# Performance work log

Hardware: AMD Instinct MI355X
Metric: run time of the kernel (lower is better)

## Reference

```python
import jax, jax.numpy as jnp
import numpy as np

N = 100000
E = 1600000
IN_C = 128
HID = 32
HEADS = 4
OUT_C = 16
G = 128
NEG_SLOPE = 0.2


def setup_inputs() -> dict:
    key = jax.random.key(0)
    ks = jax.random.split(key, 16)
    x = jax.random.normal(ks[0], (N, IN_C), dtype=jnp.float32)
    edge_index = jax.random.randint(ks[1], (2, E), 0, N, dtype=jnp.int64)
    batch = jnp.sort(jax.random.randint(ks[2], (N,), 0, G, dtype=jnp.int64))
    node_weights = jax.random.uniform(ks[3], (N, 1), dtype=jnp.float32)
    s = 1.0 / np.sqrt(IN_C)
    W1 = jax.random.uniform(ks[4], (IN_C, HEADS * HID), jnp.float32, -s, s)
    att_src1 = jax.random.uniform(ks[5], (HEADS, HID), jnp.float32, -s, s)
    att_dst1 = jax.random.uniform(ks[6], (HEADS, HID), jnp.float32, -s, s)
    b1 = jnp.zeros((HEADS * HID,), jnp.float32)
    s2 = 1.0 / np.sqrt(HEADS * HID)
    W2 = jax.random.uniform(ks[7], (HEADS * HID, HID), jnp.float32, -s2, s2)
    att_src2 = jax.random.uniform(ks[8], (1, HID), jnp.float32, -s2, s2)
    att_dst2 = jax.random.uniform(ks[9], (1, HID), jnp.float32, -s2, s2)
    b2 = jnp.zeros((HID,), jnp.float32)
    s3 = 1.0 / np.sqrt(HID)
    fcW = jax.random.uniform(ks[10], (HID, OUT_C), jnp.float32, -s3, s3)
    fcb = jax.random.uniform(ks[11], (OUT_C,), jnp.float32, -s3, s3)
    return {"x": x, "edge_index": edge_index, "batch": batch,
            "node_weights": node_weights,
            "W1": W1, "att_src1": att_src1, "att_dst1": att_dst1, "b1": b1,
            "W2": W2, "att_src2": att_src2, "att_dst2": att_dst2, "b2": b2,
            "fcW": fcW, "fcb": fcb}


def gat_conv(x, src, dst, W, att_src, att_dst, bias, heads, ch, concat):
    n = x.shape[0]
    h = (x @ W).reshape(n, heads, ch)                       # [N,H,C]
    a_src = jnp.sum(h * att_src[None], axis=-1)             # [N,H]
    a_dst = jnp.sum(h * att_dst[None], axis=-1)             # [N,H]
    e = jax.nn.leaky_relu(a_src[src] + a_dst[dst], NEG_SLOPE)  # [E,H]
    # segment softmax over incoming edges of each destination node
    e_max = jax.ops.segment_max(e, dst, num_segments=n)
    ex = jnp.exp(e - e_max[dst])
    denom = jax.ops.segment_sum(ex, dst, num_segments=n)
    alpha = ex / denom[dst]                                 # [E,H]
    msg = h[src] * alpha[..., None]                         # [E,H,C]
    out = jax.ops.segment_sum(msg, dst, num_segments=n)     # [N,H,C]
    if concat:
        out = out.reshape(n, heads * ch)
    else:
        out = out.mean(axis=1)
    return out + bias


def reference(x, edge_index, batch, node_weights,
              W1, att_src1, att_dst1, b1,
              W2, att_src2, att_dst2, b2,
              fcW, fcb):
    n = x.shape[0]
    # PyG GATConv adds self-loops by default
    loop = jnp.arange(n, dtype=edge_index.dtype)
    src = jnp.concatenate([edge_index[0], loop])
    dst = jnp.concatenate([edge_index[1], loop])

    h = x * node_weights
    h = jax.nn.elu(gat_conv(h, src, dst, W1, att_src1, att_dst1, b1, HEADS, HID, True))
    h = jax.nn.elu(gat_conv(h, src, dst, W2, att_src2, att_dst2, b2, 1, HID, False))
    # global mean pool over graphs
    sums = jax.ops.segment_sum(h, batch, num_segments=G)
    cnts = jax.ops.segment_sum(jnp.ones((n,), h.dtype), batch, num_segments=G)
    pooled = sums / jnp.maximum(cnts, 1.0)[:, None]
    return pooled @ fcW + fcb
```

## Files before the change

### kernel.cpp

```cpp
#include <hip/hip_runtime.h>
#include <cstdint>

#define NGRAPH 128
#define NEG 0.2f
#define NB_MAX 512
#define BSH 8
#define BSZ 256
#define CAP 8192

typedef unsigned int uint;
typedef unsigned short ushort;
typedef unsigned char uchar;
typedef __attribute__((ext_vector_type(8))) short bf16x8;
typedef __attribute__((ext_vector_type(4))) float f32x4;
typedef __attribute__((ext_vector_type(2))) float f32x2;

union U4B { uint4 u; bf16x8 v; };

__device__ __forceinline__ ushort f2bf(float f) {
  uint u = __float_as_uint(f);
  uint r = (u + 0x7FFF + ((u >> 16) & 1)) >> 16;
  return (ushort)r;
}

__device__ __forceinline__ uint cvtpkbf16(float lo, float hi) {
  uint r;
  asm("v_cvt_pk_bf16_f32 %0, %1, %2" : "=v"(r) : "v"(lo), "v"(hi));
  return r;
}

__device__ __forceinline__ void pkfma(f32x2& acc, f32x2 f, f32x2 w) {
  asm("v_pk_fma_f32 %0, %1, %2, %0" : "+v"(acc) : "v"(f), "v"(w));
}

__device__ __forceinline__ int wave_incl_scan_i(int v) {
  int lane = threadIdx.x & 63;
#pragma unroll
  for (int off = 1; off < 64; off <<= 1) {
    int u = __shfl_up(v, off, 64);
    if (lane >= off) v += u;
  }
  return v;
}

__global__ void k_bin(const int* __restrict__ ei,
                      const float* __restrict__ W1, const float* __restrict__ W2,
                      ushort* __restrict__ Wt1, ushort* __restrict__ Wt2,
                      int E, int Etot, int NB, int nbin,
                      int* __restrict__ bcur, uint* __restrict__ bbuf) {
  if (blockIdx.x >= (uint)nbin) {
    int t2 = (blockIdx.x - nbin) * 256 + threadIdx.x;
    if (t2 < 16384) {
      int n = t2 >> 7, k = t2 & 127;
      Wt1[t2] = f2bf(W1[k * 128 + n]);
    } else {
      int u = t2 - 16384;
      int n = u >> 7, k = u & 127;
      Wt2[u] = f2bf(W2[k * 32 + n]);
    }
    return;
  }
  __shared__ int h[NB_MAX];
  __shared__ int baseo[NB_MAX];
  int t = threadIdx.x;
  for (int b = t; b < NB; b += 256) h[b] = 0;
  __syncthreads();
  int cbase = blockIdx.x * 4096;
  int cend = min(cbase + 4096, Etot);
  for (int e = cbase + t; e < cend; e += 256) {
    int d = (e < E) ? ei[E + e] : (e - E);
    atomicAdd(&h[d >> BSH], 1);
  }
  __syncthreads();
  for (int b = t; b < NB; b += 256) {
    int c = h[b];
    baseo[b] = c ? atomicAdd(&bcur[b], c) : 0;
    h[b] = 0;
  }
  __syncthreads();
  for (int e = cbase + t; e < cend; e += 256) {
    int s, d;
    if (e < E) { s = ei[e]; d = ei[E + e]; } else { s = e - E; d = s; }
    int b = d >> BSH;
    int r = atomicAdd(&h[b], 1);
    bbuf[(size_t)b * CAP + baseo[b] + r] = ((uint)(d & (BSZ - 1)) << 17) | (uint)s;
  }
}

__global__ void k_bg(const uint* __restrict__ bbuf, const int* __restrict__ bcur,
                     int NB, int N, int* __restrict__ offs, int* __restrict__ ssrc,
                     const float* __restrict__ x, const ushort* __restrict__ Wt,
                     const float* __restrict__ nw, const float* __restrict__ att_s,
                     const float* __restrict__ att_d, uchar* __restrict__ hb1,
                     float* __restrict__ asrc, float* __restrict__ adst) {
  __shared__ int sst[NB_MAX + 1];
  __shared__ int wsum2[4];
  __shared__ int deg[BSZ];
  if (blockIdx.x < (uint)NB) {
    int t = threadIdx.x, lane = t & 63, wid = t >> 6;
    int v0 = (2 * t < NB) ? bcur[2 * t] : 0;
    int v1 = (2 * t + 1 < NB) ? bcur[2 * t + 1] : 0;
    int s = v0 + v1;
    int sv = wave_incl_scan_i(s);
    if (lane == 63) wsum2[wid] = sv;
    deg[t] = 0;
    __syncthreads();
    if (t == 0) {
      int r = 0;
#pragma unroll
      for (int k = 0; k < 4; k++) { int x2 = wsum2[k]; wsum2[k] = r; r += x2; }
    }
    __syncthreads();
    int excl = wsum2[wid] + sv - s;
    sst[2 * t] = excl;
    sst[2 * t + 1] = excl + v0;
    if (t == 255) sst[512] = excl + v0 + v1;
    __syncthreads();
    int b = blockIdx.x;
    int ebeg = sst[b], eend = sst[b + 1];
    int cnt = eend - ebeg;
    for (int i = t; i < cnt; i += BSZ)
      atomicAdd(&deg[bbuf[(size_t)b * CAP + i] >> 17], 1);
    __syncthreads();
    int v = deg[t];
    int sv2 = wave_incl_scan_i(v);
    if (lane == 63) wsum2[wid] = sv2;
    __syncthreads();
    if (t == 0) {
      int r = 0;
#pragma unroll
      for (int k = 0; k < 4; k++) { int x2 = wsum2[k]; wsum2[k] = r; r += x2; }
    }
    __syncthreads();
    int excl2 = wsum2[wid] + sv2 - v;
    int node = (b << BSH) + t;
    if (node < N) offs[node] = ebeg + excl2;
    if (b == 0 && t == 0) offs[N] = sst[512];
    __syncthreads();
    deg[t] = excl2;
    __syncthreads();
    for (int i = t; i < cnt; i += BSZ) {
      uint rec = bbuf[(size_t)b * CAP + i];
      int r = atomicAdd(&deg[rec >> 17], 1);
      ssrc[ebeg + r] = (int)(rec & 0x1FFFF);
    }
    return;
  }
  int bid = blockIdx.x - NB;
  int wv = threadIdx.x >> 6, l = threadIdx.x & 63;
  int lg = l >> 4, lr = l & 15;
  int row0 = bid * 64 + wv * 16;
  int node = row0 + lr;
  bool valid = node < N;
  float sc = valid ? nw[node] : 0.f;
  bf16x8 xfr[4];
  const float* xr = x + (size_t)node * 128;
#pragma unroll
  for (int kc = 0; kc < 4; kc++) {
    float v[8];
    if (valid) {
      float4 q0 = *reinterpret_cast<const float4*>(xr + kc * 32 + lg * 8);
      float4 q1 = *reinterpret_cast<const float4*>(xr + kc * 32 + lg * 8 + 4);
      v[0] = q0.x; v[1] = q0.y; v[2] = q0.z; v[3] = q0.w;
      v[4] = q1.x; v[5] = q1.y; v[6] = q1.z; v[7] = q1.w;
    } else {
#pragma unroll
      for (int j = 0; j < 8; j++) v[j] = 0.f;
    }
    U4B a;
    a.u.x = cvtpkbf16(v[0] * sc, v[1] * sc);
    a.u.y = cvtpkbf16(v[2] * sc, v[3] * sc);
    a.u.z = cvtpkbf16(v[4] * sc, v[5] * sc);
    a.u.w = cvtpkbf16(v[6] * sc, v[7] * sc);
    xfr[kc] = a.v;
  }
  float pS[4] = {}, pD[4] = {};
#pragma unroll
  for (int ct = 0; ct < 8; ct++) {
    f32x4 acc = {0.f, 0.f, 0.f, 0.f};
    const ushort* wrow = Wt + (size_t)(ct * 16 + lr) * 128;
#pragma unroll
    for (int kc = 0; kc < 4; kc++) {
      U4B bfr;
      bfr.u = *reinterpret_cast<const uint4*>(wrow + kc * 32 + lg * 8);
      acc = __builtin_amdgcn_mfma_f32_16x16x32_bf16(bfr.v, xfr[kc], acc, 0, 0, 0);
    }
    int c0 = ct * 16 + lg * 4;
    if (valid) {
      uint u8 = (uint)__builtin_amdgcn_cvt_pk_fp8_f32(acc[0], acc[1], 0, false);
      u8 = (uint)__builtin_amdgcn_cvt_pk_fp8_f32(acc[2], acc[3], u8, true);
      *reinterpret_cast<uint*>(hb1 + (size_t)node * 128 + c0) = u8;
    }
    float4 as4 = *reinterpret_cast<const float4*>(att_s + c0);
    float4 ad4 = *reinterpret_cast<const float4*>(att_d + c0);
    int h = ct >> 1;
    pS[h] += acc[0] * as4.x + acc[1] * as4.y + acc[2] * as4.z + acc[3] * as4.w;
    pD[h] += acc[0] * ad4.x + acc[1] * ad4.y + acc[2] * ad4.z + acc[3] * ad4.w;
  }
#pragma unroll
  for (int off = 16; off < 64; off <<= 1) {
#pragma unroll
    for (int h = 0; h < 4; h++) {
      pS[h] += __shfl_xor(pS[h], off, 64);
      pD[h] += __shfl_xor(pD[h], off, 64);
    }
  }
  if (lg == 0 && valid) {
    *reinterpret_cast<float4*>(asrc + node * 4) = make_float4(pS[0], pS[1], pS[2], pS[3]);
    *reinterpret_cast<float4*>(adst + node * 4) = make_float4(pD[0], pD[1], pD[2], pD[3]);
  }
}

__global__ void k_aggr1(const int* __restrict__ offs, const int* __restrict__ ssrc,
                        const uchar* __restrict__ hb, const float* __restrict__ asrc,
                        const float* __restrict__ adst, const float* __restrict__ bias,
                        const ushort* __restrict__ Wt2, const float* __restrict__ as2,
                        const float* __restrict__ ad2, uchar* __restrict__ hb2,
                        float* __restrict__ asrc2, float* __restrict__ adst2, int N) {
  __shared__ ushort rowl[4][136];
  int tid = threadIdx.x;
  int wv = tid >> 6, l = tid & 63;
  int d = blockIdx.x * 4 + wv;
  int dc = min(d, N - 1);
  int slot = l >> 3;
  int cb = l & 7;
  int h = cb >> 1;
  float ad = adst[dc * 4 + h];
  int beg = offs[dc], end = offs[dc + 1];
  int endm1 = end - 1;
  const uchar* hbc = hb + cb * 16;
  f32x2 a2[8] = {};
  float ds = 0.f;
  for (int i = beg; i < end; i += 8) {
    int e = i + slot;
    int ec = min(e, endm1);
    int s = ssrc[ec];
    float xv = asrc[s * 4 + h] + ad;
    xv = fmaxf(xv, xv * NEG);
    float w = __expf(xv);
    w = (e < end) ? w : 0.f;
    uint4 p = *reinterpret_cast<const uint4*>(hbc + (size_t)s * 128);
    f32x2 wp = {w, w};
    f32x2 f;
    f = __builtin_amdgcn_cvt_pk_f32_fp8(p.x, false); pkfma(a2[0], f, wp);
    f = __builtin_amdgcn_cvt_pk_f32_fp8(p.x, true);  pkfma(a2[1], f, wp);
    f = __builtin_amdgcn_cvt_pk_f32_fp8(p.y, false); pkfma(a2[2], f, wp);
    f = __builtin_amdgcn_cvt_pk_f32_fp8(p.y, true);  pkfma(a2[3], f, wp);
    f = __builtin_amdgcn_cvt_pk_f32_fp8(p.z, false); pkfma(a2[4], f, wp);
    f = __builtin_amdgcn_cvt_pk_f32_fp8(p.z, true);  pkfma(a2[5], f, wp);
    f = __builtin_amdgcn_cvt_pk_f32_fp8(p.w, false); pkfma(a2[6], f, wp);
    f = __builtin_amdgcn_cvt_pk_f32_fp8(p.w, true);  pkfma(a2[7], f, wp);
    ds += w;
  }
  int b3 = (l >> 3) & 1, b4 = (l >> 4) & 1, b5 = (l >> 5) & 1;
  float t8[8];
#pragma unroll
  for (int r = 0; r < 8; r++) {
    float av = a2[r >> 1][r & 1];
    float bv = a2[(r + 8) >> 1][r & 1];
    float send = b3 ? av : bv;
    float recv = __shfl_xor(send, 8, 64);
    t8[r] = (b3 ? bv : av) + recv;
  }
  float t4[4];
#pragma unroll
  for (int r = 0; r < 4; r++) {
    float send = b4 ? t8[r] : t8[r + 4];
    float recv = __shfl_xor(send, 16, 64);
    t4[r] = (b4 ? t8[r + 4] : t8[r]) + recv;
  }
  float t2[2];
#pragma unroll
  for (int r = 0; r < 2; r++) {
    float send = b5 ? t4[r] : t4[r + 2];
    float recv = __shfl_xor(send, 32, 64);
    t2[r] = (b5 ? t4[r + 2] : t4[r]) + recv;
  }
  ds += __shfl_xor(ds, 8, 64);
  ds += __shfl_xor(ds, 16, 64);
  ds += __shfl_xor(ds, 32, 64);
  float inv = __builtin_amdgcn_rcpf(ds > 0.f ? ds : 1.f);
  int c0 = cb * 16 + b3 * 8 + b4 * 4 + b5 * 2;
  float2 bi = *reinterpret_cast<const float2*>(bias + c0);
  float r0 = fmaf(t2[0], inv, bi.x);
  float r1 = fmaf(t2[1], inv, bi.y);
  r0 = r0 > 0.f ? r0 : __expf(r0) - 1.f;
  r1 = r1 > 0.f ? r1 : __expf(r1) - 1.f;
  *reinterpret_cast<uint*>(&rowl[wv][c0]) = cvtpkbf16(r0, r1);
  __syncthreads();
  if (wv != 0) return;
  int lg = l >> 4, lr = l & 15;
  int rsel = lr & 3;
  bf16x8 bfrag[4];
#pragma unroll
  for (int kc = 0; kc < 4; kc++) {
    U4B bb;
    bb.u = *reinterpret_cast<const uint4*>(&rowl[rsel][kc * 32 + lg * 8]);
    bfrag[kc] = bb.v;
  }
  int dd = blockIdx.x * 4 + lr;
  bool vs = (lr < 4) && (dd < N);
  float pS = 0.f, pD = 0.f;
#pragma unroll
  for (int ct = 0; ct < 2; ct++) {
    f32x4 acc = {0.f, 0.f, 0.f, 0.f};
    const ushort* wrow = Wt2 + (size_t)(ct * 16 + lr) * 128;
#pragma unroll
    for (int kc = 0; kc < 4; kc++) {
      U4B bfr;
      bfr.u = *reinterpret_cast<const uint4*>(wrow + kc * 32 + lg * 8);
      acc = __builtin_amdgcn_mfma_f32_16x16x32_bf16(bfr.v, bfrag[kc], acc, 0, 0, 0);
    }
    int cg = ct * 16 + lg * 4;
    if (vs) {
      uint u8 = (uint)__builtin_amdgcn_cvt_pk_fp8_f32(acc[0], acc[1], 0, false);
      u8 = (uint)__builtin_amdgcn_cvt_pk_fp8_f32(acc[2], acc[3], u8, true);
      *reinterpret_cast<uint*>(hb2 + (size_t)dd * 32 + cg) = u8;
    }
    float4 as4 = *reinterpret_cast<const float4*>(as2 + cg);
    float4 ad4 = *reinterpret_cast<const float4*>(ad2 + cg);
    pS += acc[0] * as4.x + acc[1] * as4.y + acc[2] * as4.z + acc[3] * as4.w;
    pD += acc[0] * ad4.x + acc[1] * ad4.y + acc[2] * ad4.z + acc[3] * ad4.w;
  }
  pS += __shfl_xor(pS, 16, 64);
  pS += __shfl_xor(pS, 32, 64);
  pD += __shfl_xor(pD, 16, 64);
  pD += __shfl_xor(pD, 32, 64);
  if (vs && lg == 0) { asrc2[dd] = pS; adst2[dd] = pD; }
}

__global__ void k_aggr2(const int* __restrict__ offs, const int* __restrict__ ssrc,
                        const uchar* __restrict__ hb, const float* __restrict__ asrc,
                        const float* __restrict__ adst, const float* __restrict__ bias,
                        float* __restrict__ out, int N) {
  int wid = threadIdx.x >> 6, l = threadIdx.x & 63;
  int d = blockIdx.x * 4 + wid;
  if (d >= N) return;
  int slot = l >> 2;
  int k = l & 3;
  float ad = adst[d];
  int beg = offs[d], end = offs[d + 1];
  int endm1 = end - 1;
  const uchar* hbc = hb + k * 8;
  f32x2 a2[4] = {};
  float ds = 0.f;
  for (int i = beg; i < end; i += 16) {
    int e = i + slot;
    int ec = min(e, endm1);
    int s = ssrc[ec];
    float xv = asrc[s] + ad;
    xv = fmaxf(xv, xv * NEG);
    float w = __expf(xv);
    w = (e < end) ? w : 0.f;
    uint2 p = *reinterpret_cast<const uint2*>(hbc + (size_t)s * 32);
    f32x2 wp = {w, w};
    f32x2 f;
    f = __builtin_amdgcn_cvt_pk_f32_fp8(p.x, false); pkfma(a2[0], f, wp);
    f = __builtin_amdgcn_cvt_pk_f32_fp8(p.x, true);  pkfma(a2[1], f, wp);
    f = __builtin_amdgcn_cvt_pk_f32_fp8(p.y, false); pkfma(a2[2], f, wp);
    f = __builtin_amdgcn_cvt_pk_f32_fp8(p.y, true);  pkfma(a2[3], f, wp);
    ds += w;
  }
  int b2 = (l >> 2) & 1, b3 = (l >> 3) & 1, b4 = (l >> 4) & 1;
  float t4[4];
#pragma unroll
  for (int r = 0; r < 4; r++) {
    float av = a2[r >> 1][r & 1];
    float bv = a2[(r + 4) >> 1][r & 1];
    float send = b2 ? av : bv;
    float recv = __shfl_xor(send, 4, 64);
    t4[r] = (b2 ? bv : av) + recv;
  }
  float t2[2];
#pragma unroll
  for (int r = 0; r < 2; r++) {
    float send = b3 ? t4[r] : t4[r + 2];
    float recv = __shfl_xor(send, 8, 64);
    t2[r] = (b3 ? t4[r + 2] : t4[r]) + recv;
  }
  float send = b4 ? t2[0] : t2[1];
  float recv = __shfl_xor(send, 16, 64);
  float t1 = (b4 ? t2[1] : t2[0]) + recv;
  t1 += __shfl_xor(t1, 32, 64);
  ds += __shfl_xor(ds, 4, 64);
  ds += __shfl_xor(ds, 8, 64);
  ds += __shfl_xor(ds, 16, 64);
  ds += __shfl_xor(ds, 32, 64);
  if (l < 32) {
    int c = k * 8 + b2 * 4 + b3 * 2 + b4;
    float inv = __builtin_amdgcn_rcpf(ds > 0.f ? ds : 1.f);
    float r = fmaf(t1, inv, bias[c]);
    r = r > 0.f ? r : __expf(r) - 1.f;
    out[(size_t)d * 32 + c] = r;
  }
}

__global__ void k_pool_fc(const float* __restrict__ h2, const int* __restrict__ batch,
                          const float* __restrict__ fcW, const float* __restrict__ fcb,
                          float* __restrict__ out, int N) {
  int g = blockIdx.x;
  int lo = 0, hi = N;
  while (lo < hi) { int mid = (lo + hi) >> 1; if (batch[mid] < g) lo = mid + 1; else hi = mid; }
  int beg = lo;
  hi = N;
  while (lo < hi) { int mid = (lo + hi) >> 1; if (batch[mid] < g + 1) lo = mid + 1; else hi = mid; }
  int end = lo;
  int t = threadIdx.x, c = t & 31, sub = t >> 5;
  float acc = 0.f;
  for (int n = beg + sub; n < end; n += 8) acc += h2[(size_t)n * 32 + c];
  __shared__ float red[8][32];
  __shared__ float pooled[32];
  red[sub][c] = acc;
  __syncthreads();
  if (sub == 0) {
    float s = 0.f;
#pragma unroll
    for (int i = 0; i < 8; i++) s += red[i][c];
    float cnt = (float)(end - beg);
    pooled[c] = s / fmaxf(cnt, 1.f);
  }
  __syncthreads();
  if (t < 16) {
    float r = fcb[t];
#pragma unroll
    for (int cc = 0; cc < 32; cc++) r += pooled[cc] * fcW[cc * 16 + t];
    out[g * 16 + t] = r;
  }
}

extern "C" void kernel_launch(void* const* d_in, const int* in_sizes, int n_in,
                              void* d_out, int out_size, void* d_ws, size_t ws_size,
                              hipStream_t stream) {
  const float* x     = (const float*)d_in[0];
  const int*   ei    = (const int*)d_in[1];
  const int*   batch = (const int*)d_in[2];
  const float* nw    = (const float*)d_in[3];
  const float* W1    = (const float*)d_in[4];
  const float* as1w  = (const float*)d_in[5];
  const float* ad1w  = (const float*)d_in[6];
  const float* b1    = (const float*)d_in[7];
  const float* W2    = (const float*)d_in[8];
  const float* as2w  = (const float*)d_in[9];
  const float* ad2w  = (const float*)d_in[10];
  const float* b2    = (const float*)d_in[11];
  const float* fcW   = (const float*)d_in[12];
  const float* fcb   = (const float*)d_in[13];
  float* out = (float*)d_out;

  const int N = in_sizes[0] / 128;
  const int E = in_sizes[1] / 2;
  const int Etot = E + N;
  const int NB = (N + BSZ - 1) >> BSH;

  char* w = (char*)d_ws;
  size_t ofs = 0;
  auto alloc = [&](size_t bytes) {
    char* p = w + ofs;
    ofs += (bytes + 255) & ~(size_t)255;
    return p;
  };
  uchar*  hb1    = (uchar*)alloc((size_t)N * 128);
  uchar*  hb2    = (uchar*)alloc((size_t)N * 32);
  float*  h2     = (float*)alloc((size_t)N * 32 * 4);
  float*  asrc1  = (float*)alloc((size_t)N * 4 * 4);
  float*  adst1  = (float*)alloc((size_t)N * 4 * 4);
  float*  asrc2  = (float*)alloc((size_t)N * 4);
  float*  adst2  = (float*)alloc((size_t)N * 4);
  ushort* Wt1    = (ushort*)alloc(16384 * 2);
  ushort* Wt2    = (ushort*)alloc(4096 * 2);
  int*    bcur   = (int*)alloc((size_t)NB * 4);
  int*    offs   = (int*)alloc((size_t)(N + 1) * 4);
  uint*   bbuf   = (uint*)alloc((size_t)NB * CAP * 4);
  int*    ssrc   = (int*)alloc((size_t)Etot * 4);

  hipMemsetAsync(bcur, 0, (size_t)NB * 4, stream);

  const int nbin = (Etot + 4095) / 4096;
  k_bin<<<nbin + 80, 256, 0, stream>>>(ei, W1, W2, Wt1, Wt2, E, Etot, NB, nbin, bcur, bbuf);

  const int ngemm1 = (N + 63) / 64;
  k_bg<<<NB + ngemm1, 256, 0, stream>>>(bbuf, bcur, NB, N, offs, ssrc,
                                        x, Wt1, nw, as1w, ad1w, hb1, asrc1, adst1);

  k_aggr1<<<(N + 3) / 4, 256, 0, stream>>>(offs, ssrc, hb1, asrc1, adst1, b1,
                                           Wt2, as2w, ad2w, hb2, asrc2, adst2, N);

  k_aggr2<<<(N + 3) / 4, 256, 0, stream>>>(offs, ssrc, hb2, asrc2, adst2, b2, h2, N);

  k_pool_fc<<<NGRAPH, 256, 0, stream>>>(h2, batch, fcW, fcb, out, N);
}
```

Baseline: 308.9 us.

## Compute edge weights once per edge and broadcast via ds_bpermute in aggregation

Both aggregation kernels now load source indices and compute the leaky-relu and exp attention weight once per edge per head, using dedicated lanes. The weights and indices are then broadcast to the lanes that do the feature gathers with ds_bpermute, instead of every lane redundantly loading ssrc/asrc and computing exp. Each iteration processes 32 (layer 1) or 64 (layer 2) edges, with up to four gathers in flight per lane. This removes redundant scalar loads and transcendental work and raises memory-level parallelism, at the cost of extra LDS permute traffic and branches for the tail chunks.

After: 305.1 us. About the same (-1.2%).

```diff
diff --git a/kernel.cpp b/kernel.cpp
--- a/kernel.cpp
+++ b/kernel.cpp
@@ -31,6 +31,13 @@
 
 __device__ __forceinline__ void pkfma(f32x2& acc, f32x2 f, f32x2 w) {
   asm("v_pk_fma_f32 %0, %1, %2, %0" : "+v"(acc) : "v"(f), "v"(w));
+}
+
+__device__ __forceinline__ float bperm_f(int addr, float v) {
+  return __int_as_float(__builtin_amdgcn_ds_bpermute(addr, __float_as_int(v)));
+}
+__device__ __forceinline__ int bperm_i(int addr, int v) {
+  return __builtin_amdgcn_ds_bpermute(addr, v);
 }
 
 __device__ __forceinline__ int wave_incl_scan_i(int v) {
@@ -225,21 +232,17 @@
   int slot = l >> 3;
   int cb = l & 7;
   int h = cb >> 1;
-  float ad = adst[dc * 4 + h];
+  int hq = l & 3;
+  int eidx = l >> 2;
+  float adq = adst[dc * 4 + hq];
   int beg = offs[dc], end = offs[dc + 1];
   int endm1 = end - 1;
   const uchar* hbc = hb + cb * 16;
+  int bp0 = (slot * 4 + h) << 2;
+  int bp1 = bp0 + 128;
   f32x2 a2[8] = {};
-  float ds = 0.f;
-  for (int i = beg; i < end; i += 8) {
-    int e = i + slot;
-    int ec = min(e, endm1);
-    int s = ssrc[ec];
-    float xv = asrc[s * 4 + h] + ad;
-    xv = fmaxf(xv, xv * NEG);
-    float w = __expf(xv);
-    w = (e < end) ? w : 0.f;
-    uint4 p = *reinterpret_cast<const uint4*>(hbc + (size_t)s * 128);
+  float dsp = 0.f;
+  auto ACC = [&](uint4 p, float w) {
     f32x2 wp = {w, w};
     f32x2 f;
     f = __builtin_amdgcn_cvt_pk_f32_fp8(p.x, false); pkfma(a2[0], f, wp);
@@ -250,8 +253,43 @@
     f = __builtin_amdgcn_cvt_pk_f32_fp8(p.z, true);  pkfma(a2[5], f, wp);
     f = __builtin_amdgcn_cvt_pk_f32_fp8(p.w, false); pkfma(a2[6], f, wp);
     f = __builtin_amdgcn_cvt_pk_f32_fp8(p.w, true);  pkfma(a2[7], f, wp);
-    ds += w;
-  }
+  };
+  for (int base = beg; base < end; base += 32) {
+    int eA = base + eidx;
+    int eB = eA + 16;
+    int sA = ssrc[min(eA, endm1)];
+    int sB = ssrc[min(eB, endm1)];
+    int s0 = bperm_i(bp0, sA);
+    int s1 = bperm_i(bp1, sA);
+    int s2 = bperm_i(bp0, sB);
+    int s3 = bperm_i(bp1, sB);
+    int rem = end - base;
+    uint4 p0, p1, p2, p3;
+    p0 = *reinterpret_cast<const uint4*>(hbc + (size_t)s0 * 128);
+    if (rem > 8)  p1 = *reinterpret_cast<const uint4*>(hbc + (size_t)s1 * 128);
+    if (rem > 16) p2 = *reinterpret_cast<const uint4*>(hbc + (size_t)s2 * 128);
+    if (rem > 24) p3 = *reinterpret_cast<const uint4*>(hbc + (size_t)s3 * 128);
+    float aA = asrc[sA * 4 + hq] + adq;
+    float aB = asrc[sB * 4 + hq] + adq;
+    aA = fmaxf(aA, aA * NEG);
+    aB = fmaxf(aB, aB * NEG);
+    float wA = (eA < end) ? __expf(aA) : 0.f;
+    float wB = (eB < end) ? __expf(aB) : 0.f;
+    dsp += wA + wB;
+    float w0 = bperm_f(bp0, wA);
+    float w1 = bperm_f(bp1, wA);
+    float w2 = bperm_f(bp0, wB);
+    float w3 = bperm_f(bp1, wB);
+    ACC(p0, w0);
+    if (rem > 8)  ACC(p1, w1);
+    if (rem > 16) ACC(p2, w2);
+    if (rem > 24) ACC(p3, w3);
+  }
+  dsp += __shfl_xor(dsp, 4, 64);
+  dsp += __shfl_xor(dsp, 8, 64);
+  dsp += __shfl_xor(dsp, 16, 64);
+  dsp += __shfl_xor(dsp, 32, 64);
+  float ds = bperm_f(h << 2, dsp);
   int b3 = (l >> 3) & 1, b4 = (l >> 4) & 1, b5 = (l >> 5) & 1;
   float t8[8];
 #pragma unroll
@@ -276,9 +314,6 @@
     float recv = __shfl_xor(send, 32, 64);
     t2[r] = (b5 ? t4[r + 2] : t4[r]) + recv;
   }
-  ds += __shfl_xor(ds, 8, 64);
-  ds += __shfl_xor(ds, 16, 64);
-  ds += __shfl_xor(ds, 32, 64);
   float inv = __builtin_amdgcn_rcpf(ds > 0.f ? ds : 1.f);
   int c0 = cb * 16 + b3 * 8 + b4 * 4 + b5 * 2;
   float2 bi = *reinterpret_cast<const float2*>(bias + c0);
@@ -342,25 +377,52 @@
   int beg = offs[d], end = offs[d + 1];
   int endm1 = end - 1;
   const uchar* hbc = hb + k * 8;
+  int bq0 = slot << 2;
+  int bq1 = (slot + 16) << 2;
+  int bq2 = (slot + 32) << 2;
+  int bq3 = (slot + 48) << 2;
   f32x2 a2[4] = {};
-  float ds = 0.f;
-  for (int i = beg; i < end; i += 16) {
-    int e = i + slot;
-    int ec = min(e, endm1);
-    int s = ssrc[ec];
-    float xv = asrc[s] + ad;
-    xv = fmaxf(xv, xv * NEG);
-    float w = __expf(xv);
-    w = (e < end) ? w : 0.f;
-    uint2 p = *reinterpret_cast<const uint2*>(hbc + (size_t)s * 32);
+  float dsp = 0.f;
+  auto ACC2 = [&](uint2 p, float w) {
     f32x2 wp = {w, w};
     f32x2 f;
     f = __builtin_amdgcn_cvt_pk_f32_fp8(p.x, false); pkfma(a2[0], f, wp);
     f = __builtin_amdgcn_cvt_pk_f32_fp8(p.x, true);  pkfma(a2[1], f, wp);
     f = __builtin_amdgcn_cvt_pk_f32_fp8(p.y, false); pkfma(a2[2], f, wp);
     f = __builtin_amdgcn_cvt_pk_f32_fp8(p.y, true);  pkfma(a2[3], f, wp);
-    ds += w;
-  }
+  };
+  for (int base = beg; base < end; base += 64) {
+    int e = base + l;
+    int sL = ssrc[min(e, endm1)];
+    int s0 = bperm_i(bq0, sL);
+    int s1 = bperm_i(bq1, sL);
+    int s2 = bperm_i(bq2, sL);
+    int s3 = bperm_i(bq3, sL);
+    int rem = end - base;
+    uint2 p0, p1, p2, p3;
+    p0 = *reinterpret_cast<const uint2*>(hbc + (size_t)s0 * 32);
+    if (rem > 16) p1 = *reinterpret_cast<const uint2*>(hbc + (size_t)s1 * 32);
+    if (rem > 32) p2 = *reinterpret_cast<const uint2*>(hbc + (size_t)s2 * 32);
+    if (rem > 48) p3 = *reinterpret_cast<const uint2*>(hbc + (size_t)s3 * 32);
+    float xv = asrc[sL] + ad;
+    xv = fmaxf(xv, xv * NEG);
+    float wL = (e < end) ? __expf(xv) : 0.f;
+    dsp += wL;
+    float w0 = bperm_f(bq0, wL);
+    float w1 = bperm_f(bq1, wL);
+    float w2 = bperm_f(bq2, wL);
+    float w3 = bperm_f(bq3, wL);
+    ACC2(p0, w0);
+    if (rem > 16) ACC2(p1, w1);
+    if (rem > 32) ACC2(p2, w2);
+    if (rem > 48) ACC2(p3, w3);
+  }
+  dsp += __shfl_xor(dsp, 1, 64);
+  dsp += __shfl_xor(dsp, 2, 64);
+  dsp += __shfl_xor(dsp, 4, 64);
+  dsp += __shfl_xor(dsp, 8, 64);
+  dsp += __shfl_xor(dsp, 16, 64);
+  dsp += __shfl_xor(dsp, 32, 64);
   int b2 = (l >> 2) & 1, b3 = (l >> 3) & 1, b4 = (l >> 4) & 1;
   float t4[4];
 #pragma unroll
@@ -382,13 +444,9 @@
   float recv = __shfl_xor(send, 16, 64);
   float t1 = (b4 ? t2[1] : t2[0]) + recv;
   t1 += __shfl_xor(t1, 32, 64);
-  ds += __shfl_xor(ds, 4, 64);
-  ds += __shfl_xor(ds, 8, 64);
-  ds += __shfl_xor(ds, 16, 64);
-  ds += __shfl_xor(ds, 32, 64);
   if (l < 32) {
     int c = k * 8 + b2 * 4 + b3 * 2 + b4;
-    float inv = __builtin_amdgcn_rcpf(ds > 0.f ? ds : 1.f);
+    float inv = __builtin_amdgcn_rcpf(dsp > 0.f ? dsp : 1.f);
     float r = fmaf(t1, inv, bias[c]);
     r = r > 0.f ? r : __expf(r) - 1.f;
     out[(size_t)d * 32 + c] = r;
```
